# Kernel optimization log

Measured on AMD Instinct MI355X. Metric: run time of the kernel, lower is better.

## Reference

```python
import jax, jax.numpy as jnp
import numpy as np

ANGSTROM_TO_BOHR = 1.8897261258369282
CUTOFF = 5.2  # angstrom
N_SPECIES = 4  # H, C, N, O

# GFN1-xTB-style per-element constants for (H, C, N, O)
_ALPHA = np.array([2.209700, 1.247655, 1.524329, 1.845886], dtype=np.float32)
_Y_EFF = np.array([1.116244, 4.428763, 5.498808, 5.171786], dtype=np.float32)


def _smooth_cutoff(d, rc, eps=1e-10):
    # torchani 'smooth' cutoff: exp(1 - 1/(1 - (d/rc)^2)) for d < rc, else 0
    x2 = (d / rc) ** 2
    e = 1.0 - 1.0 / jnp.maximum(1.0 - x2, eps)
    return jnp.where(d < rc, jnp.exp(e), jnp.zeros_like(d))


def setup_inputs() -> dict:
    key = jax.random.key(0)
    k1, k2, k3 = jax.random.split(key, 3)
    M, A, P = 2048, 64, 8388608
    element_idxs = jax.random.randint(k1, (M, A), 0, N_SPECIES, dtype=jnp.int64)
    neighbor_idxs = jax.random.randint(k2, (2, P), 0, M * A, dtype=jnp.int64)
    distances = jax.random.uniform(k3, (P,), dtype=jnp.float32, minval=0.5, maxval=6.0)
    # precomputed pairwise parameter tables (buffers in the torch module)
    y_ab = jnp.asarray(np.outer(_Y_EFF, _Y_EFF))                 # [4,4]
    sqrt_alpha_ab = jnp.asarray(np.sqrt(np.outer(_ALPHA, _ALPHA)))  # [4,4]
    k_rep = np.full((N_SPECIES, N_SPECIES), 1.5, dtype=np.float32)
    k_rep[0, 0] = 1.0  # H-H
    k_rep_ab = jnp.asarray(k_rep)
    return {
        "element_idxs": element_idxs,
        "neighbor_idxs": neighbor_idxs,
        "distances": distances,
        "y_ab": y_ab,
        "sqrt_alpha_ab": sqrt_alpha_ab,
        "k_rep_ab": k_rep_ab,
    }


def reference(element_idxs, neighbor_idxs, distances, y_ab, sqrt_alpha_ab, k_rep_ab):
    M, A = element_idxs.shape
    d = jnp.clip(distances, 1e-7) * ANGSTROM_TO_BOHR  # [P] bohr
    species12 = element_idxs.reshape(-1)[neighbor_idxs]  # [2, P]
    s0, s1 = species12[0], species12[1]
    y = y_ab[s0, s1]                    # [P] gather
    sa = sqrt_alpha_ab[s0, s1]          # [P]
    kr = k_rep_ab[s0, s1]               # [P]
    rep = (y / d) * jnp.exp(-sa * d ** kr)
    rep = rep * _smooth_cutoff(d, CUTOFF * ANGSTROM_TO_BOHR)
    mol_idx = neighbor_idxs[0] // A     # [P]
    energies = jax.ops.segment_sum(rep, mol_idx, num_segments=M)  # [M]
    return energies
```

## Files before the change

kernel.cpp:

```cpp
#include <hip/hip_runtime.h>


#define AB_D 1.8897261258369282
#define L2E  1.4426950408889634f

__global__ __launch_bounds__(256) void pack_zero_kernel(
    const int* __restrict__ elem, int natoms, int nwords,
    unsigned* __restrict__ packed, float* __restrict__ out, int M)
{
    int g = blockIdx.x * blockDim.x + threadIdx.x;
    if (g < M) out[g] = 0.0f;
    if (packed != nullptr && g < nwords) {
        int base = g * 16;
        unsigned w = 0u;
        if (base + 16 <= natoms) {
            const int4* p = (const int4*)(elem + base);
            #pragma unroll
            for (int q = 0; q < 4; ++q) {
                int4 v = p[q];
                w |= ((unsigned)v.x & 3u) << (2 * (4 * q + 0));
                w |= ((unsigned)v.y & 3u) << (2 * (4 * q + 1));
                w |= ((unsigned)v.z & 3u) << (2 * (4 * q + 2));
                w |= ((unsigned)v.w & 3u) << (2 * (4 * q + 3));
            }
        } else {
            for (int j = 0; j < 16; ++j) {
                int a = base + j;
                unsigned s = (a < natoms) ? ((unsigned)elem[a] & 3u) : 0u;
                w |= s << (2 * j);
            }
        }
        packed[g] = w;
    }
}

__global__ __launch_bounds__(1024, 8) void rep_main_kernel(
    const int* __restrict__ nbr, const float* __restrict__ dist,
    const unsigned* __restrict__ packed_g,
    const float* __restrict__ y_ab, const float* __restrict__ sa_ab,
    const float* __restrict__ kr_ab,
    long long P, int M, int nwords, unsigned long long molMagic, int A,
    float* __restrict__ partials, float* __restrict__ out,
    int mode )
{
    extern __shared__ char smem[];
    float*  acc = (float*)smem;
    float2* tbl = (float2*)(smem + (size_t)M * 4);
    unsigned* pk = (unsigned*)(smem + (size_t)M * 4 + 16 * sizeof(float2));

    const int tid = threadIdx.x;
    const int nthr = blockDim.x;

    for (int m = tid; m < M; m += nthr) acc[m] = 0.0f;
    {
        int nw4 = nwords >> 2;
        const uint4* src4 = (const uint4*)packed_g;
        uint4* dst4 = (uint4*)pk;
        for (int w = tid; w < nw4; w += nthr) dst4[w] = src4[w];
        for (int w = (nw4 << 2) + tid; w < nwords; w += nthr) pk[w] = packed_g[w];
    }
    if (tid < 16) {
        float sa = sa_ab[tid] * L2E;
        if (kr_ab[tid] == 1.0f) sa = -sa;
        tbl[tid] = make_float2(y_ab[tid], sa);
    }
    __syncthreads();

    const float ABf   = (float)AB_D;
    const float DMIN  = (float)(1e-7 * AB_D);
    const float RCINV = (float)(1.0 / (5.2 * AB_D));

    const int4*   nb04 = (const int4*)nbr;
    const int4*   nb14 = (const int4*)(nbr + P);
    const float4* dv4  = (const float4*)dist;

    auto pair = [&](unsigned ua0, unsigned ua1, float draw) {
        unsigned w0 = pk[ua0 >> 4];
        unsigned w1 = pk[ua1 >> 4];
        unsigned s0 = (w0 >> ((ua0 & 15u) * 2u)) & 3u;
        unsigned s1 = (w1 >> ((ua1 & 15u) * 2u)) & 3u;
        float2 t = tbl[s0 * 4u + s1];
        float d   = fmaxf(draw * ABf, DMIN);
        float x   = d * RCINV;
        float om  = fmaxf(fmaf(-x, x, 1.0f), 0.0f);
        float r   = __builtin_amdgcn_rcpf(om);
        float e   = fmaf(-L2E, r, L2E);
        float sq  = __builtin_amdgcn_sqrtf(d);
        float fac = (t.y < 0.0f) ? 1.0f : sq;
        float arg = fmaf(-fabsf(t.y), d * fac, e);
        float ex  = __builtin_amdgcn_exp2f(arg);
        float rep = t.x * __builtin_amdgcn_rcpf(d) * ex;
        unsigned mol = (unsigned)(((unsigned long long)ua0 * molMagic) >> 42);
        atomicAdd(&acc[mol], rep);
    };

    auto process = [&](int4 i0, int4 i1, float4 dv) {
        pair((unsigned)i0.x, (unsigned)i1.x, dv.x);
        pair((unsigned)i0.y, (unsigned)i1.y, dv.y);
        pair((unsigned)i0.z, (unsigned)i1.z, dv.z);
        pair((unsigned)i0.w, (unsigned)i1.w, dv.w);
    };

    long long P4 = P >> 2;
    long long gstride = (long long)gridDim.x * nthr;
    long long mega = gstride << 2;

    for (long long i = (long long)blockIdx.x * nthr + tid; i < P4; i += mega) {
        long long j1 = i + gstride, j2 = i + 2 * gstride, j3 = i + 3 * gstride;
        if (j3 < P4) {
            int4   A0 = nb04[i];  int4   A1 = nb04[j1];
            int4   A2 = nb04[j2]; int4   A3 = nb04[j3];
            int4   B0 = nb14[i];  int4   B1 = nb14[j1];
            int4   B2 = nb14[j2]; int4   B3 = nb14[j3];
            float4 D0 = dv4[i];   float4 D1 = dv4[j1];
            float4 D2 = dv4[j2];  float4 D3 = dv4[j3];
            __builtin_amdgcn_sched_barrier(0);
            process(A0, B0, D0);
            process(A1, B1, D1);
            process(A2, B2, D2);
            process(A3, B3, D3);
        } else {
            for (long long j = i; j < P4; j += gstride)
                process(nb04[j], nb14[j], dv4[j]);
        }
    }

    long long tail0 = P4 << 2;
    if (blockIdx.x == 0) {
        const int* nb0 = nbr;
        const int* nb1 = nbr + P;
        for (long long p = tail0 + tid; p < P; p += nthr)
            pair((unsigned)nb0[p], (unsigned)nb1[p], dist[p]);
    }
    __syncthreads();

    if (mode == 0) {
        float* row = partials + (size_t)blockIdx.x * (size_t)M;
        for (int m = tid; m < M; m += nthr) row[m] = acc[m];
    } else {
        for (int m = tid; m < M; m += nthr) {
            float v = acc[m];
            if (v != 0.0f) atomicAdd(&out[m], v);
        }
    }
}

__global__ __launch_bounds__(256) void reduce_kernel(
    const float* __restrict__ partials, float* __restrict__ out,
    int M, int nblk, int rows_per)
{
    int m = blockIdx.x * blockDim.x + threadIdx.x;
    if (m >= M) return;
    int r0 = blockIdx.y * rows_per;
    int r1 = r0 + rows_per;
    if (r1 > nblk) r1 = nblk;
    if (r0 >= r1) return;
    float s0 = 0.f, s1 = 0.f, s2 = 0.f, s3 = 0.f;
    int r = r0;
    for (; r + 3 < r1; r += 4) {
        s0 += partials[(size_t)(r + 0) * M + m];
        s1 += partials[(size_t)(r + 1) * M + m];
        s2 += partials[(size_t)(r + 2) * M + m];
        s3 += partials[(size_t)(r + 3) * M + m];
    }
    for (; r < r1; ++r) s0 += partials[(size_t)r * M + m];
    atomicAdd(&out[m], (s0 + s1) + (s2 + s3));
}

extern "C" void kernel_launch(void* const* d_in, const int* in_sizes, int n_in,
                              void* d_out, int out_size, void* d_ws, size_t ws_size,
                              hipStream_t stream)
{
    const int*   elem  = (const int*)d_in[0];
    const int*   nbr   = (const int*)d_in[1];
    const float* dist  = (const float*)d_in[2];
    const float* y_ab  = (const float*)d_in[3];
    const float* sa_ab = (const float*)d_in[4];
    const float* kr_ab = (const float*)d_in[5];
    float* out = (float*)d_out;

    const int natoms = in_sizes[0];
    const long long P = (long long)in_sizes[2];
    const int M = out_size;
    const int A = natoms / M;
    unsigned long long molMagic =
        (A > 0) ? ((((unsigned long long)1 << 42) + (unsigned long long)A - 1)
                   / (unsigned long long)A)
                : 1ull;
    const int nwords = (natoms + 15) / 16;

    size_t packed_bytes = ((size_t)nwords * 4 + 255) & ~(size_t)255;
    bool have_packed = (ws_size >= packed_bytes);
    unsigned* packed = have_packed ? (unsigned*)d_ws : nullptr;
    if (!have_packed) return;

    const int BLOCK = 1024;
    int nblk = 512;
    float* partials = nullptr;
    int mode = 1;
    {
        size_t avail = ws_size - packed_bytes;
        size_t rowb = (size_t)M * 4;
        long long maxrows = (long long)(avail / rowb);
        if (maxrows >= 64) {
            nblk = (int)(maxrows < 512 ? maxrows : 512);
            partials = (float*)((char*)d_ws + packed_bytes);
            mode = 0;
        }
    }

    {
        int total = (nwords > M) ? nwords : M;
        int g = (total + 255) / 256;
        hipLaunchKernelGGL(pack_zero_kernel, dim3(g), dim3(256), 0, stream,
                           elem, natoms, nwords, packed, out, M);
    }

    {
        size_t smem = (size_t)M * 4 + 16 * sizeof(float2) + (size_t)nwords * 4;
        hipLaunchKernelGGL(rep_main_kernel, dim3(nblk), dim3(BLOCK), smem, stream,
                           nbr, dist, packed, y_ab, sa_ab, kr_ab,
                           P, M, nwords, molMagic, A, partials, out, mode);
    }

    if (mode == 0) {
        const int SPLIT = 32;
        int rows_per = (nblk + SPLIT - 1) / SPLIT;
        dim3 grid((M + 255) / 256, SPLIT);
        hipLaunchKernelGGL(reduce_kernel, grid, dim3(256), 0, stream,
                           partials, out, M, nblk, rows_per);
    }
}
```

Baseline: 156.0 us.

## Split pair loop across two sequential kernels with different block shapes

The single main kernel is split into two launches. The first uses 1024-thread blocks with a simple grid-stride loop over the first half of the pairs. The second uses 512-thread blocks with the 4-way batched-load loop over the second half, and adds its per-block partials onto the rows the first kernel wrote. Both kernels reload the packed species table and zero the shared accumulators, which adds launch and setup cost, and the simple loop in the first kernel gives up the batched memory-level parallelism.

```diff
diff --git a/kernel.cpp b/kernel.cpp
--- a/kernel.cpp
+++ b/kernel.cpp
@@ -34,79 +34,136 @@
     }
 }
 
-__global__ __launch_bounds__(1024, 8) void rep_main_kernel(
+struct SmemView {
+    float* acc;
+    float2* tbl;
+    unsigned* pk;
+};
+
+__device__ inline SmemView smem_init(
+    char* smem, int M, int nwords, int tid, int nthr,
+    const unsigned* packed_g, const float* y_ab, const float* sa_ab,
+    const float* kr_ab)
+{
+    SmemView v;
+    v.acc = (float*)smem;
+    v.tbl = (float2*)(smem + (size_t)M * 4);
+    v.pk  = (unsigned*)(smem + (size_t)M * 4 + 16 * sizeof(float2));
+    for (int m = tid; m < M; m += nthr) v.acc[m] = 0.0f;
+    int nw4 = nwords >> 2;
+    const uint4* src4 = (const uint4*)packed_g;
+    uint4* dst4 = (uint4*)v.pk;
+    for (int w = tid; w < nw4; w += nthr) dst4[w] = src4[w];
+    for (int w = (nw4 << 2) + tid; w < nwords; w += nthr) v.pk[w] = packed_g[w];
+    if (tid < 16) {
+        float sa = sa_ab[tid] * L2E;
+        if (kr_ab[tid] == 1.0f) sa = -sa;
+        v.tbl[tid] = make_float2(y_ab[tid], sa);
+    }
+    __syncthreads();
+    return v;
+}
+
+__device__ inline void pair_op(
+    const SmemView& v, unsigned ua0, unsigned ua1, float draw,
+    unsigned long long molMagic)
+{
+    const float ABf   = (float)AB_D;
+    const float DMIN  = (float)(1e-7 * AB_D);
+    const float RCINV = (float)(1.0 / (5.2 * AB_D));
+    unsigned w0 = v.pk[ua0 >> 4];
+    unsigned w1 = v.pk[ua1 >> 4];
+    unsigned s0 = (w0 >> ((ua0 & 15u) * 2u)) & 3u;
+    unsigned s1 = (w1 >> ((ua1 & 15u) * 2u)) & 3u;
+    float2 t = v.tbl[s0 * 4u + s1];
+    float d   = fmaxf(draw * ABf, DMIN);
+    float x   = d * RCINV;
+    float om  = fmaxf(fmaf(-x, x, 1.0f), 0.0f);
+    float r   = __builtin_amdgcn_rcpf(om);
+    float e   = fmaf(-L2E, r, L2E);
+    float sq  = __builtin_amdgcn_sqrtf(d);
+    float fac = (t.y < 0.0f) ? 1.0f : sq;
+    float arg = fmaf(-fabsf(t.y), d * fac, e);
+    float ex  = __builtin_amdgcn_exp2f(arg);
+    float rep = t.x * __builtin_amdgcn_rcpf(d) * ex;
+    unsigned mol = (unsigned)(((unsigned long long)ua0 * molMagic) >> 42);
+    atomicAdd(&v.acc[mol], rep);
+}
+
+__global__ __launch_bounds__(1024, 8) void rep_main_a(
     const int* __restrict__ nbr, const float* __restrict__ dist,
     const unsigned* __restrict__ packed_g,
     const float* __restrict__ y_ab, const float* __restrict__ sa_ab,
     const float* __restrict__ kr_ab,
-    long long P, int M, int nwords, unsigned long long molMagic, int A,
-    float* __restrict__ partials, float* __restrict__ out,
-    int mode )
+    long long P, long long split, int M, int nwords,
+    unsigned long long molMagic,
+    float* __restrict__ partials, float* __restrict__ out, int mode)
 {
     extern __shared__ char smem[];
-    float*  acc = (float*)smem;
-    float2* tbl = (float2*)(smem + (size_t)M * 4);
-    unsigned* pk = (unsigned*)(smem + (size_t)M * 4 + 16 * sizeof(float2));
-
     const int tid = threadIdx.x;
     const int nthr = blockDim.x;
-
-    for (int m = tid; m < M; m += nthr) acc[m] = 0.0f;
-    {
-        int nw4 = nwords >> 2;
-        const uint4* src4 = (const uint4*)packed_g;
-        uint4* dst4 = (uint4*)pk;
-        for (int w = tid; w < nw4; w += nthr) dst4[w] = src4[w];
-        for (int w = (nw4 << 2) + tid; w < nwords; w += nthr) pk[w] = packed_g[w];
-    }
-    if (tid < 16) {
-        float sa = sa_ab[tid] * L2E;
-        if (kr_ab[tid] == 1.0f) sa = -sa;
-        tbl[tid] = make_float2(y_ab[tid], sa);
-    }
-    __syncthreads();
-
-    const float ABf   = (float)AB_D;
-    const float DMIN  = (float)(1e-7 * AB_D);
-    const float RCINV = (float)(1.0 / (5.2 * AB_D));
+    SmemView v = smem_init(smem, M, nwords, tid, nthr, packed_g, y_ab, sa_ab, kr_ab);
 
     const int4*   nb04 = (const int4*)nbr;
     const int4*   nb14 = (const int4*)(nbr + P);
     const float4* dv4  = (const float4*)dist;
 
-    auto pair = [&](unsigned ua0, unsigned ua1, float draw) {
-        unsigned w0 = pk[ua0 >> 4];
-        unsigned w1 = pk[ua1 >> 4];
-        unsigned s0 = (w0 >> ((ua0 & 15u) * 2u)) & 3u;
-        unsigned s1 = (w1 >> ((ua1 & 15u) * 2u)) & 3u;
-        float2 t = tbl[s0 * 4u + s1];
-        float d   = fmaxf(draw * ABf, DMIN);
-        float x   = d * RCINV;
-        float om  = fmaxf(fmaf(-x, x, 1.0f), 0.0f);
-        float r   = __builtin_amdgcn_rcpf(om);
-        float e   = fmaf(-L2E, r, L2E);
-        float sq  = __builtin_amdgcn_sqrtf(d);
-        float fac = (t.y < 0.0f) ? 1.0f : sq;
-        float arg = fmaf(-fabsf(t.y), d * fac, e);
-        float ex  = __builtin_amdgcn_exp2f(arg);
-        float rep = t.x * __builtin_amdgcn_rcpf(d) * ex;
-        unsigned mol = (unsigned)(((unsigned long long)ua0 * molMagic) >> 42);
-        atomicAdd(&acc[mol], rep);
-    };
-
-    auto process = [&](int4 i0, int4 i1, float4 dv) {
-        pair((unsigned)i0.x, (unsigned)i1.x, dv.x);
-        pair((unsigned)i0.y, (unsigned)i1.y, dv.y);
-        pair((unsigned)i0.z, (unsigned)i1.z, dv.z);
-        pair((unsigned)i0.w, (unsigned)i1.w, dv.w);
-    };
+    long long gstride = (long long)gridDim.x * nthr;
+    for (long long i = (long long)blockIdx.x * nthr + tid; i < split; i += gstride) {
+        int4   i0 = nb04[i];
+        int4   i1 = nb14[i];
+        float4 dv = dv4[i];
+        pair_op(v, (unsigned)i0.x, (unsigned)i1.x, dv.x, molMagic);
+        pair_op(v, (unsigned)i0.y, (unsigned)i1.y, dv.y, molMagic);
+        pair_op(v, (unsigned)i0.z, (unsigned)i1.z, dv.z, molMagic);
+        pair_op(v, (unsigned)i0.w, (unsigned)i1.w, dv.w, molMagic);
+    }
 
     long long P4 = P >> 2;
-    long long gstride = (long long)gridDim.x * nthr;
-    long long mega = gstride << 2;
-
-    for (long long i = (long long)blockIdx.x * nthr + tid; i < P4; i += mega) {
-        long long j1 = i + gstride, j2 = i + 2 * gstride, j3 = i + 3 * gstride;
+    long long tail0 = P4 << 2;
+    if (blockIdx.x == 0) {
+        const int* nb0 = nbr;
+        const int* nb1 = nbr + P;
+        for (long long p = tail0 + tid; p < P; p += nthr)
+            pair_op(v, (unsigned)nb0[p], (unsigned)nb1[p], dist[p], molMagic);
+    }
+    __syncthreads();
+
+    if (mode == 0) {
+        float* row = partials + (size_t)blockIdx.x * (size_t)M;
+        for (int m = tid; m < M; m += nthr) row[m] = v.acc[m];
+    } else {
+        for (int m = tid; m < M; m += nthr) {
+            float val = v.acc[m];
+            if (val != 0.0f) atomicAdd(&out[m], val);
+        }
+    }
+}
+
+__global__ __launch_bounds__(512, 4) void rep_main_b(
+    const int* __restrict__ nbr, const float* __restrict__ dist,
+    const unsigned* __restrict__ packed_g,
+    const float* __restrict__ y_ab, const float* __restrict__ sa_ab,
+    const float* __restrict__ kr_ab,
+    long long P, long long split, int M, int nwords,
+    unsigned long long molMagic,
+    float* __restrict__ partials, float* __restrict__ out, int mode)
+{
+    extern __shared__ char smem[];
+    const int tid = threadIdx.x;
+    const int nthr = blockDim.x;
+    SmemView v = smem_init(smem, M, nwords, tid, nthr, packed_g, y_ab, sa_ab, kr_ab);
+
+    const int4*   nb04 = (const int4*)nbr;
+    const int4*   nb14 = (const int4*)(nbr + P);
+    const float4* dv4  = (const float4*)dist;
+
+    long long P4 = P >> 2;
+    long long g = (long long)gridDim.x * nthr;
+    long long mega = g << 2;
+
+    for (long long i = split + (long long)blockIdx.x * nthr + tid; i < P4; i += mega) {
+        long long j1 = i + g, j2 = i + 2 * g, j3 = i + 3 * g;
         if (j3 < P4) {
             int4   A0 = nb04[i];  int4   A1 = nb04[j1];
             int4   A2 = nb04[j2]; int4   A3 = nb04[j3];
@@ -115,32 +172,43 @@
             float4 D0 = dv4[i];   float4 D1 = dv4[j1];
             float4 D2 = dv4[j2];  float4 D3 = dv4[j3];
             __builtin_amdgcn_sched_barrier(0);
-            process(A0, B0, D0);
-            process(A1, B1, D1);
-            process(A2, B2, D2);
-            process(A3, B3, D3);
+            pair_op(v, (unsigned)A0.x, (unsigned)B0.x, D0.x, molMagic);
+            pair_op(v, (unsigned)A0.y, (unsigned)B0.y, D0.y, molMagic);
+            pair_op(v, (unsigned)A0.z, (unsigned)B0.z, D0.z, molMagic);
+            pair_op(v, (unsigned)A0.w, (unsigned)B0.w, D0.w, molMagic);
+            pair_op(v, (unsigned)A1.x, (unsigned)B1.x, D1.x, molMagic);
+            pair_op(v, (unsigned)A1.y, (unsigned)B1.y, D1.y, molMagic);
+            pair_op(v, (unsigned)A1.z, (unsigned)B1.z, D1.z, molMagic);
+            pair_op(v, (unsigned)A1.w, (unsigned)B1.w, D1.w, molMagic);
+            pair_op(v, (unsigned)A2.x, (unsigned)B2.x, D2.x, molMagic);
+            pair_op(v, (unsigned)A2.y, (unsigned)B2.y, D2.y, molMagic);
+            pair_op(v, (unsigned)A2.z, (unsigned)B2.z, D2.z, molMagic);
+            pair_op(v, (unsigned)A2.w, (unsigned)B2.w, D2.w, molMagic);
+            pair_op(v, (unsigned)A3.x, (unsigned)B3.x, D3.x, molMagic);
+            pair_op(v, (unsigned)A3.y, (unsigned)B3.y, D3.y, molMagic);
+            pair_op(v, (unsigned)A3.z, (unsigned)B3.z, D3.z, molMagic);
+            pair_op(v, (unsigned)A3.w, (unsigned)B3.w, D3.w, molMagic);
         } else {
-            for (long long j = i; j < P4; j += gstride)
-                process(nb04[j], nb14[j], dv4[j]);
-        }
-    }
-
-    long long tail0 = P4 << 2;
-    if (blockIdx.x == 0) {
-        const int* nb0 = nbr;
-        const int* nb1 = nbr + P;
-        for (long long p = tail0 + tid; p < P; p += nthr)
-            pair((unsigned)nb0[p], (unsigned)nb1[p], dist[p]);
+            for (long long j = i; j < P4; j += g) {
+                int4   i0 = nb04[j];
+                int4   i1 = nb14[j];
+                float4 dv = dv4[j];
+                pair_op(v, (unsigned)i0.x, (unsigned)i1.x, dv.x, molMagic);
+                pair_op(v, (unsigned)i0.y, (unsigned)i1.y, dv.y, molMagic);
+                pair_op(v, (unsigned)i0.z, (unsigned)i1.z, dv.z, molMagic);
+                pair_op(v, (unsigned)i0.w, (unsigned)i1.w, dv.w, molMagic);
+            }
+        }
     }
     __syncthreads();
 
     if (mode == 0) {
         float* row = partials + (size_t)blockIdx.x * (size_t)M;
-        for (int m = tid; m < M; m += nthr) row[m] = acc[m];
+        for (int m = tid; m < M; m += nthr) row[m] += v.acc[m];
     } else {
         for (int m = tid; m < M; m += nthr) {
-            float v = acc[m];
-            if (v != 0.0f) atomicAdd(&out[m], v);
+            float val = v.acc[m];
+            if (val != 0.0f) atomicAdd(&out[m], val);
         }
     }
 }
@@ -194,7 +262,6 @@
     unsigned* packed = have_packed ? (unsigned*)d_ws : nullptr;
     if (!have_packed) return;
 
-    const int BLOCK = 1024;
     int nblk = 512;
     float* partials = nullptr;
     int mode = 1;
@@ -209,6 +276,9 @@
         }
     }
 
+    long long P4 = P >> 2;
+    long long split = P4 >> 1;
+
     {
         int total = (nwords > M) ? nwords : M;
         int g = (total + 255) / 256;
@@ -216,12 +286,15 @@
                            elem, natoms, nwords, packed, out, M);
     }
 
-    {
-        size_t smem = (size_t)M * 4 + 16 * sizeof(float2) + (size_t)nwords * 4;
-        hipLaunchKernelGGL(rep_main_kernel, dim3(nblk), dim3(BLOCK), smem, stream,
-                           nbr, dist, packed, y_ab, sa_ab, kr_ab,
-                           P, M, nwords, molMagic, A, partials, out, mode);
-    }
+    size_t smem = (size_t)M * 4 + 16 * sizeof(float2) + (size_t)nwords * 4;
+
+    hipLaunchKernelGGL(rep_main_a, dim3(nblk), dim3(1024), smem, stream,
+                       nbr, dist, packed, y_ab, sa_ab, kr_ab,
+                       P, split, M, nwords, molMagic, partials, out, mode);
+
+    hipLaunchKernelGGL(rep_main_b, dim3(nblk), dim3(512), smem, stream,
+                       nbr, dist, packed, y_ab, sa_ab, kr_ab,
+                       P, split, M, nwords, molMagic, partials, out, mode);
 
     if (mode == 0) {
         const int SPLIT = 32;
```

Result: slower. 169.9 us (+8.9%).
